# Optimization experiments

Hardware: AMD Instinct MI355X
Metric: run time of the kernel (lower is better)

The kernel has to match this reference:

```python
import jax, jax.numpy as jnp
import numpy as np

ALPHA = 32.0
LN_EPS = 1e-5

def _cdist(a, b):
    # a: [C, M, K], b: [C, N, K] -> [C, M, N] euclidean distances
    d2 = (jnp.sum(a * a, -1)[:, :, None]
          + jnp.sum(b * b, -1)[:, None, :]
          - 2.0 * jnp.einsum('cmk,cnk->cmn', a, b))
    return jnp.sqrt(jnp.maximum(d2, 1e-12))

def setup_inputs() -> dict:
    key = jax.random.key(0)
    k1, k2 = jax.random.split(key)
    B, D, H, W, C = 8, 16, 28, 28, 256
    CN, SS = 128, 28 * 28
    x = jax.random.normal(k1, (B, D, H, W, C), dtype=jnp.float32)
    ln_weight = jnp.ones((C,), dtype=jnp.float32)
    ln_bias = jnp.zeros((C,), dtype=jnp.float32)
    cluster_center = jax.random.uniform(k2, (C, CN, SS), dtype=jnp.float32)
    return {"x": x, "ln_weight": ln_weight, "ln_bias": ln_bias,
            "cluster_center": cluster_center}

def reference(x, ln_weight, ln_bias, cluster_center):
    B, D, H, W, C = x.shape
    CN = cluster_center.shape[1]
    # LayerNorm over last dim (feature_dim)
    mu = jnp.mean(x, -1, keepdims=True)
    var = jnp.mean(jnp.square(x - mu), -1, keepdims=True)
    xn = (x - mu) * jax.lax.rsqrt(var + LN_EPS) * ln_weight + ln_bias
    # B D H W C -> C (B D) (H W)
    x_re = jnp.transpose(xn, (4, 0, 1, 2, 3)).reshape(C, B * D, H * W)
    soft_assign = _cdist(x_re, cluster_center)          # [C, B*D, CN]
    # C (B D) CN -> B D C CN
    x_distance = jnp.transpose(soft_assign.reshape(C, B, D, CN), (1, 2, 0, 3))
    # NegSoftAssign: exp(-alpha*(x - min)) normalized == softmax(-alpha*x)
    x_distance_assign = jax.nn.softmax(-ALPHA * x_distance, axis=-1)
    cluster_dist = _cdist(cluster_center, cluster_center)  # [C, CN, CN]
    return (x_distance, x_distance_assign, cluster_dist)
```

## Files before the change

kernel.cpp:

```cpp
#include <hip/hip_runtime.h>
#include <hip/hip_bf16.h>
#include <math.h>

#define C_DIM 256
#define BD    128
#define HW    784
#define CN    128
#define KPAD  800

typedef short bf16x8 __attribute__((ext_vector_type(8)));
typedef float f32x4 __attribute__((ext_vector_type(4)));

__device__ inline ushort f2b(float f) {
  unsigned u = __float_as_uint(f);
  unsigned r = (u + 0x7FFFu + ((u >> 16) & 1u)) >> 16;
  return (ushort)r;
}

__global__ __launch_bounds__(256) void ln_transpose_kernel(
    const float* __restrict__ x, const float* __restrict__ lnw,
    const float* __restrict__ lnb, ushort* __restrict__ xre,
    float* __restrict__ anorm) {
  __shared__ ushort btile[256 * 36];
  __shared__ float nbuf[4][256];
  const int t = threadIdx.x, bd = blockIdx.y, bx = blockIdx.x;
  const int hw0 = bx * 32;
  const int w = t >> 6, lane = t & 63;
  const int q = lane >> 4, l = lane & 15;
  const bool last = (bx == 24);
  const int ngroups = last ? 1 : 2;
  const int rpw = ngroups * 4;
  if (last) {
    for (int r = 16; r < 32; ++r) btile[t * 36 + r] = 0;
  }
  float4 wv[4], bv[4];
  for (int s = 0; s < 4; ++s) {
    wv[s] = *(const float4*)(lnw + s * 64 + l * 4);
    bv[s] = *(const float4*)(lnb + s * 64 + l * 4);
  }
  float nrm[4][4];
  for (int s = 0; s < 4; ++s)
    for (int j = 0; j < 4; ++j) nrm[s][j] = 0.f;
  const float* xb = x + ((size_t)bd * HW + hw0) * 256 + l * 4;
  for (int g = 0; g < ngroups; ++g) {
    int r = w * rpw + g * 4 + q;
    float4 v[4];
    for (int s = 0; s < 4; ++s)
      v[s] = *(const float4*)(xb + (size_t)r * 256 + s * 64);
    float sum = 0.f, sq = 0.f;
    for (int s = 0; s < 4; ++s) {
      sum += v[s].x + v[s].y + v[s].z + v[s].w;
      sq = fmaf(v[s].x, v[s].x, sq); sq = fmaf(v[s].y, v[s].y, sq);
      sq = fmaf(v[s].z, v[s].z, sq); sq = fmaf(v[s].w, v[s].w, sq);
    }
    for (int off = 1; off <= 8; off <<= 1) {
      sum += __shfl_xor(sum, off, 64);
      sq  += __shfl_xor(sq, off, 64);
    }
    float mu = sum * (1.f / 256.f);
    float var = fmaf(-mu, mu, sq * (1.f / 256.f));
    float sc = rsqrtf(var + 1e-5f);
    for (int s = 0; s < 4; ++s) {
      float y0 = (v[s].x - mu) * sc * wv[s].x + bv[s].x;
      float y1 = (v[s].y - mu) * sc * wv[s].y + bv[s].y;
      float y2 = (v[s].z - mu) * sc * wv[s].z + bv[s].z;
      float y3 = (v[s].w - mu) * sc * wv[s].w + bv[s].w;
      nrm[s][0] = fmaf(y0, y0, nrm[s][0]);
      nrm[s][1] = fmaf(y1, y1, nrm[s][1]);
      nrm[s][2] = fmaf(y2, y2, nrm[s][2]);
      nrm[s][3] = fmaf(y3, y3, nrm[s][3]);
      int c = s * 64 + l * 4;
      btile[(c + 0) * 36 + r] = f2b(y0);
      btile[(c + 1) * 36 + r] = f2b(y1);
      btile[(c + 2) * 36 + r] = f2b(y2);
      btile[(c + 3) * 36 + r] = f2b(y3);
    }
  }
  for (int s = 0; s < 4; ++s)
    for (int j = 0; j < 4; ++j) {
      float v = nrm[s][j];
      v += __shfl_xor(v, 16, 64);
      v += __shfl_xor(v, 32, 64);
      nrm[s][j] = v;
    }
  if (q == 0)
    for (int s = 0; s < 4; ++s)
      for (int j = 0; j < 4; ++j) nbuf[w][s * 64 + l * 4 + j] = nrm[s][j];
  __syncthreads();
  float tot = nbuf[0][t] + nbuf[1][t] + nbuf[2][t] + nbuf[3][t];
  atomicAdd(&anorm[t * 128 + bd], tot);
  for (int i = 0; i < 8; ++i) {
    int c = w * 64 + i * 8 + (lane >> 3);
    int ho = (lane & 7) * 4;
    ushort4 val = *(const ushort4*)&btile[c * 36 + ho];
    *(ushort4*)(xre + (size_t)c * (BD * KPAD) + (size_t)bd * KPAD + hw0 + ho) = val;
  }
}

__global__ __launch_bounds__(256) void cc_convert_kernel(
    const float* __restrict__ cc, ushort* __restrict__ ccb,
    float* __restrict__ bnorm) {
  int b = blockIdx.x, c = b >> 3;
  int t = threadIdx.x, w = t >> 6, lane = t & 63;
  int q = lane >> 4, l = lane & 15;
  int r = (b & 7) * 16 + w * 4 + q;
  const float4* src = (const float4*)(cc + ((size_t)c * CN + r) * HW);
  ushort* dst = ccb + ((size_t)c * CN + r) * KPAD;
  float nrm = 0.f;
  for (int i = 0; i < 13; ++i) {
    int f = i * 16 + l;
    if (f < 196) {
      float4 v = src[f];
      nrm = fmaf(v.x, v.x, nrm); nrm = fmaf(v.y, v.y, nrm);
      nrm = fmaf(v.z, v.z, nrm); nrm = fmaf(v.w, v.w, nrm);
      ushort4 o; o.x = f2b(v.x); o.y = f2b(v.y); o.z = f2b(v.z); o.w = f2b(v.w);
      *(ushort4*)(dst + f * 4) = o;
    }
  }
  for (int off = 1; off <= 8; off <<= 1) nrm += __shfl_xor(nrm, off, 64);
  if (l == 0) bnorm[c * 128 + r] = nrm;
  if (l < 4) *(ushort4*)(dst + 784 + l * 4) = make_ushort4(0, 0, 0, 0);
}

__global__ __launch_bounds__(256, 2) void gemm_mfma_kernel(
    const ushort* __restrict__ xre, const ushort* __restrict__ ccb,
    const float* __restrict__ anorm, const float* __restrict__ bnorm,
    float* __restrict__ out_d, float* __restrict__ out_s,
    float* __restrict__ out_c) {
  __shared__ __align__(16) ushort At[2][4096];
  __shared__ __align__(16) ushort Bt[2][4096];
  __shared__ float smin[2][128];
  __shared__ float ssum[2][128];
  const int bx = blockIdx.x;
  const int c = bx >> 1, mode = bx & 1;
  const int t = threadIdx.x, w = t >> 6, lane = t & 63;
  const int quad = lane >> 4, ln = lane & 15;
  const int wrow = (w >> 1) * 64, wcol = (w & 1) * 64;
  const ushort* Ag = (mode ? ccb : xre) + (size_t)c * (128 * KPAD);
  const ushort* Bg = ccb + (size_t)c * (128 * KPAD);

  f32x4 acc[4][4];
  for (int i = 0; i < 4; ++i)
    for (int j = 0; j < 4; ++j) acc[i][j] = f32x4{0.f, 0.f, 0.f, 0.f};

  const int ci0 = 128 * w;
  const int row0 = (ci0 + lane) >> 2;
  const int row1 = (ci0 + 64 + lane) >> 2;
  const int q0 = (lane & 3) ^ (row0 & 3);
  const int q1 = (lane & 3) ^ (row1 & 3);
  const ushort* ga0 = Ag + (size_t)row0 * KPAD + q0 * 8;
  const ushort* ga1 = Ag + (size_t)row1 * KPAD + q1 * 8;
  const ushort* gb0 = Bg + (size_t)row0 * KPAD + q0 * 8;
  const ushort* gb1 = Bg + (size_t)row1 * KPAD + q1 * 8;
  const int la0 = ci0 * 8, la1 = (ci0 + 64) * 8;

#define ISSUE(k, p)                                                          \
  do {                                                                       \
    int kb = (k) * 32;                                                       \
    __builtin_amdgcn_global_load_lds(                                        \
        (const __attribute__((address_space(1))) unsigned int*)(ga0 + kb),   \
        (__attribute__((address_space(3))) unsigned int*)&At[p][la0], 16, 0, 0); \
    __builtin_amdgcn_global_load_lds(                                        \
        (const __attribute__((address_space(1))) unsigned int*)(ga1 + kb),   \
        (__attribute__((address_space(3))) unsigned int*)&At[p][la1], 16, 0, 0); \
    if (!mode) {                                                             \
      __builtin_amdgcn_global_load_lds(                                      \
          (const __attribute__((address_space(1))) unsigned int*)(gb0 + kb), \
          (__attribute__((address_space(3))) unsigned int*)&Bt[p][la0], 16, 0, 0); \
      __builtin_amdgcn_global_load_lds(                                      \
          (const __attribute__((address_space(1))) unsigned int*)(gb1 + kb), \
          (__attribute__((address_space(3))) unsigned int*)&Bt[p][la1], 16, 0, 0); \
    }                                                                        \
  } while (0)

  ISSUE(0, 0);
  for (int k0 = 0; k0 < 25; ++k0) {
    __syncthreads();
    if (k0 < 24) ISSUE(k0 + 1, (k0 + 1) & 1);
    const ushort* Ab = At[k0 & 1];
    const ushort* Bb = mode ? At[k0 & 1] : Bt[k0 & 1];
    bf16x8 af[4], bf[4];
    for (int i = 0; i < 4; ++i) {
      int m = wrow + i * 16 + ln;
      af[i] = *(const bf16x8*)&Ab[(m * 4 + (quad ^ (m & 3))) * 8];
    }
    for (int j = 0; j < 4; ++j) {
      int n = wcol + j * 16 + ln;
      bf[j] = *(const bf16x8*)&Bb[(n * 4 + (quad ^ (n & 3))) * 8];
    }
    for (int i = 0; i < 4; ++i)
      for (int j = 0; j < 4; ++j)
        acc[i][j] = __builtin_amdgcn_mfma_f32_16x16x32_bf16(af[i], bf[j], acc[i][j], 0, 0, 0);
  }
#undef ISSUE

  const float* rn = (mode ? bnorm : anorm) + c * 128;
  const float* cn = bnorm + c * 128;
  float cnv[4];
  for (int j = 0; j < 4; ++j) cnv[j] = cn[wcol + j * 16 + ln];
  float d[4][4][4];
  for (int i = 0; i < 4; ++i) {
    float rv[4];
    for (int r = 0; r < 4; ++r) rv[r] = rn[wrow + i * 16 + quad * 4 + r];
    for (int j = 0; j < 4; ++j)
      for (int r = 0; r < 4; ++r) {
        float d2 = rv[r] + cnv[j] - 2.f * acc[i][j][r];
        d[i][j][r] = sqrtf(fmaxf(d2, 1e-12f));
      }
  }

  if (mode) {
    float* ob = out_c + (size_t)c * (128 * 128);
    for (int i = 0; i < 4; ++i)
      for (int r = 0; r < 4; ++r) {
        int m = wrow + i * 16 + quad * 4 + r;
        for (int j = 0; j < 4; ++j) ob[m * 128 + wcol + j * 16 + ln] = d[i][j][r];
      }
  } else {
    int half = w & 1;
    for (int i = 0; i < 4; ++i)
      for (int r = 0; r < 4; ++r) {
        int m = wrow + i * 16 + quad * 4 + r;
        size_t ob = ((size_t)m * 256 + c) * 128 + wcol;
        for (int j = 0; j < 4; ++j) out_d[ob + j * 16 + ln] = d[i][j][r];
        float mn = fminf(fminf(d[i][0][r], d[i][1][r]), fminf(d[i][2][r], d[i][3][r]));
        for (int off = 1; off < 16; off <<= 1) mn = fminf(mn, __shfl_xor(mn, off, 64));
        if (ln == 0) smin[half][m] = mn;
      }
    __syncthreads();
    for (int i = 0; i < 4; ++i)
      for (int r = 0; r < 4; ++r) {
        int m = wrow + i * 16 + quad * 4 + r;
        float mn = fminf(smin[0][m], smin[1][m]);
        float s = 0.f;
        for (int j = 0; j < 4; ++j) {
          float e = __expf(-32.f * (d[i][j][r] - mn));
          d[i][j][r] = e;
          s += e;
        }
        for (int off = 1; off < 16; off <<= 1) s += __shfl_xor(s, off, 64);
        if (ln == 0) ssum[half][m] = s;
      }
    __syncthreads();
    for (int i = 0; i < 4; ++i)
      for (int r = 0; r < 4; ++r) {
        int m = wrow + i * 16 + quad * 4 + r;
        float inv = 1.f / (ssum[0][m] + ssum[1][m]);
        size_t ob = ((size_t)m * 256 + c) * 128 + wcol;
        for (int j = 0; j < 4; ++j) out_s[ob + j * 16 + ln] = d[i][j][r] * inv;
      }
  }
}

extern "C" void kernel_launch(void* const* d_in, const int* in_sizes, int n_in,
                              void* d_out, int out_size, void* d_ws, size_t ws_size,
                              hipStream_t stream) {
  const float* x   = (const float*)d_in[0];
  const float* lnw = (const float*)d_in[1];
  const float* lnb = (const float*)d_in[2];
  const float* cc  = (const float*)d_in[3];
  float* out   = (float*)d_out;
  float* out_d = out;
  float* out_s = out + 4194304;
  float* out_c = out + 8388608;

  ushort* xre_b = (ushort*)d_ws;
  ushort* cc_b  = xre_b + 26214400;
  float*  anorm = (float*)(cc_b + 26214400);
  float*  bnorm = anorm + 32768;

  hipMemsetAsync(anorm, 0, 32768 * sizeof(float), stream);
  ln_transpose_kernel<<<dim3(25, 128), 256, 0, stream>>>(x, lnw, lnb, xre_b, anorm);
  cc_convert_kernel<<<2048, 256, 0, stream>>>(cc, cc_b, bnorm);
  gemm_mfma_kernel<<<512, 256, 0, stream>>>(xre_b, cc_b, anorm, bnorm,
                                            out_d, out_s, out_c);
}
```

Measured before the change: 320.0 us.

## Split GEMM tiles by column half, move softmax to separate kernel, widen LN tiles

The GEMM grid doubles by giving each block half of the cluster columns. This cuts accumulators and shared memory so occupancy can rise to 4 blocks per CU, and 1024 blocks run instead of 512. The fused softmax, with its cross-wave min and sum reductions, moves into a separate row-wise kernel that re-reads out_d from global memory. The LN/transpose kernel now handles 64 spatial positions per block with an XOR-swizzled shared tile, and K is padded to 832. These changes trade an extra full read and write pass over the distance tensor for better GEMM parallelism and simpler epilogues.

```diff
diff --git a/kernel.cpp b/kernel.cpp
--- a/kernel.cpp
+++ b/kernel.cpp
@@ -6,7 +6,8 @@
 #define BD    128
 #define HW    784
 #define CN    128
-#define KPAD  800
+#define KPAD  832
+#define KTILES 26
 
 typedef short bf16x8 __attribute__((ext_vector_type(8)));
 typedef float f32x4 __attribute__((ext_vector_type(4)));
@@ -21,17 +22,18 @@
     const float* __restrict__ x, const float* __restrict__ lnw,
     const float* __restrict__ lnb, ushort* __restrict__ xre,
     float* __restrict__ anorm) {
-  __shared__ ushort btile[256 * 36];
+  __shared__ ushort btile[256 * 64];
   __shared__ float nbuf[4][256];
   const int t = threadIdx.x, bd = blockIdx.y, bx = blockIdx.x;
-  const int hw0 = bx * 32;
+  const int hw0 = bx * 64;
   const int w = t >> 6, lane = t & 63;
   const int q = lane >> 4, l = lane & 15;
-  const bool last = (bx == 24);
-  const int ngroups = last ? 1 : 2;
+  const bool last = (bx == 12);
+  const int ngroups = last ? 1 : 4;
   const int rpw = ngroups * 4;
   if (last) {
-    for (int r = 16; r < 32; ++r) btile[t * 36 + r] = 0;
+    for (int r = 16; r < 64; r += 4)
+      *(ushort4*)&btile[t * 64 + r] = make_ushort4(0, 0, 0, 0);
   }
   float4 wv[4], bv[4];
   for (int s = 0; s < 4; ++s) {
@@ -42,6 +44,7 @@
   for (int s = 0; s < 4; ++s)
     for (int j = 0; j < 4; ++j) nrm[s][j] = 0.f;
   const float* xb = x + ((size_t)bd * HW + hw0) * 256 + l * 4;
+  const int xr = l & 12;
   for (int g = 0; g < ngroups; ++g) {
     int r = w * rpw + g * 4 + q;
     float4 v[4];
@@ -60,6 +63,7 @@
     float mu = sum * (1.f / 256.f);
     float var = fmaf(-mu, mu, sq * (1.f / 256.f));
     float sc = rsqrtf(var + 1e-5f);
+    int rp = r ^ xr;
     for (int s = 0; s < 4; ++s) {
       float y0 = (v[s].x - mu) * sc * wv[s].x + bv[s].x;
       float y1 = (v[s].y - mu) * sc * wv[s].y + bv[s].y;
@@ -70,10 +74,10 @@
       nrm[s][2] = fmaf(y2, y2, nrm[s][2]);
       nrm[s][3] = fmaf(y3, y3, nrm[s][3]);
       int c = s * 64 + l * 4;
-      btile[(c + 0) * 36 + r] = f2b(y0);
-      btile[(c + 1) * 36 + r] = f2b(y1);
-      btile[(c + 2) * 36 + r] = f2b(y2);
-      btile[(c + 3) * 36 + r] = f2b(y3);
+      btile[(c + 0) * 64 + rp] = f2b(y0);
+      btile[(c + 1) * 64 + rp] = f2b(y1);
+      btile[(c + 2) * 64 + rp] = f2b(y2);
+      btile[(c + 3) * 64 + rp] = f2b(y3);
     }
   }
   for (int s = 0; s < 4; ++s)
@@ -89,11 +93,12 @@
   __syncthreads();
   float tot = nbuf[0][t] + nbuf[1][t] + nbuf[2][t] + nbuf[3][t];
   atomicAdd(&anorm[t * 128 + bd], tot);
-  for (int i = 0; i < 8; ++i) {
-    int c = w * 64 + i * 8 + (lane >> 3);
-    int ho = (lane & 7) * 4;
-    ushort4 val = *(const ushort4*)&btile[c * 36 + ho];
-    *(ushort4*)(xre + (size_t)c * (BD * KPAD) + (size_t)bd * KPAD + hw0 + ho) = val;
+  for (int i = 0; i < 16; ++i) {
+    int c = w * 64 + i * 4 + (lane >> 4);
+    int xw = (w * 16 + i) & 12;
+    int ho = (lane & 15) * 4;
+    uint2 val = *(const uint2*)&btile[c * 64 + (ho ^ xw)];
+    *(uint2*)(xre + (size_t)c * (BD * KPAD) + (size_t)bd * KPAD + hw0 + ho) = val;
   }
 }
 
@@ -119,137 +124,121 @@
   }
   for (int off = 1; off <= 8; off <<= 1) nrm += __shfl_xor(nrm, off, 64);
   if (l == 0) bnorm[c * 128 + r] = nrm;
-  if (l < 4) *(ushort4*)(dst + 784 + l * 4) = make_ushort4(0, 0, 0, 0);
-}
-
-__global__ __launch_bounds__(256, 2) void gemm_mfma_kernel(
+  if (l < 12) *(ushort4*)(dst + 784 + l * 4) = make_ushort4(0, 0, 0, 0);
+}
+
+__global__ __launch_bounds__(256, 4) void gemm_mfma_kernel(
     const ushort* __restrict__ xre, const ushort* __restrict__ ccb,
     const float* __restrict__ anorm, const float* __restrict__ bnorm,
-    float* __restrict__ out_d, float* __restrict__ out_s,
-    float* __restrict__ out_c) {
+    float* __restrict__ out_d, float* __restrict__ out_c) {
   __shared__ __align__(16) ushort At[2][4096];
-  __shared__ __align__(16) ushort Bt[2][4096];
-  __shared__ float smin[2][128];
-  __shared__ float ssum[2][128];
+  __shared__ __align__(16) ushort Bt[2][2048];
   const int bx = blockIdx.x;
-  const int c = bx >> 1, mode = bx & 1;
+  const int c = bx >> 2, mode = (bx >> 1) & 1, nh = bx & 1;
   const int t = threadIdx.x, w = t >> 6, lane = t & 63;
   const int quad = lane >> 4, ln = lane & 15;
-  const int wrow = (w >> 1) * 64, wcol = (w & 1) * 64;
   const ushort* Ag = (mode ? ccb : xre) + (size_t)c * (128 * KPAD);
-  const ushort* Bg = ccb + (size_t)c * (128 * KPAD);
-
-  f32x4 acc[4][4];
-  for (int i = 0; i < 4; ++i)
+  const ushort* Bg = ccb + (size_t)c * (128 * KPAD) + (size_t)(nh * 64) * KPAD;
+
+  f32x4 acc[2][4];
+  for (int i = 0; i < 2; ++i)
     for (int j = 0; j < 4; ++j) acc[i][j] = f32x4{0.f, 0.f, 0.f, 0.f};
 
-  const int ci0 = 128 * w;
-  const int row0 = (ci0 + lane) >> 2;
-  const int row1 = (ci0 + 64 + lane) >> 2;
-  const int q0 = (lane & 3) ^ (row0 & 3);
-  const int q1 = (lane & 3) ^ (row1 & 3);
-  const ushort* ga0 = Ag + (size_t)row0 * KPAD + q0 * 8;
-  const ushort* ga1 = Ag + (size_t)row1 * KPAD + q1 * 8;
-  const ushort* gb0 = Bg + (size_t)row0 * KPAD + q0 * 8;
-  const ushort* gb1 = Bg + (size_t)row1 * KPAD + q1 * 8;
-  const int la0 = ci0 * 8, la1 = (ci0 + 64) * 8;
-
-#define ISSUE(k, p)                                                          \
-  do {                                                                       \
-    int kb = (k) * 32;                                                       \
-    __builtin_amdgcn_global_load_lds(                                        \
-        (const __attribute__((address_space(1))) unsigned int*)(ga0 + kb),   \
-        (__attribute__((address_space(3))) unsigned int*)&At[p][la0], 16, 0, 0); \
-    __builtin_amdgcn_global_load_lds(                                        \
-        (const __attribute__((address_space(1))) unsigned int*)(ga1 + kb),   \
-        (__attribute__((address_space(3))) unsigned int*)&At[p][la1], 16, 0, 0); \
-    if (!mode) {                                                             \
-      __builtin_amdgcn_global_load_lds(                                      \
-          (const __attribute__((address_space(1))) unsigned int*)(gb0 + kb), \
-          (__attribute__((address_space(3))) unsigned int*)&Bt[p][la0], 16, 0, 0); \
-      __builtin_amdgcn_global_load_lds(                                      \
-          (const __attribute__((address_space(1))) unsigned int*)(gb1 + kb), \
-          (__attribute__((address_space(3))) unsigned int*)&Bt[p][la1], 16, 0, 0); \
-    }                                                                        \
+  const int ciA0 = w * 128 + lane, ciA1 = ciA0 + 64;
+  const int rowA0 = ciA0 >> 2, rowA1 = ciA1 >> 2;
+  const int qA0 = (ciA0 & 3) ^ (rowA0 & 3), qA1 = (ciA1 & 3) ^ (rowA1 & 3);
+  const ushort* gA0 = Ag + (size_t)rowA0 * KPAD + qA0 * 8;
+  const ushort* gA1 = Ag + (size_t)rowA1 * KPAD + qA1 * 8;
+  const int rowB = t >> 2, qB = (t & 3) ^ (rowB & 3);
+  const ushort* gB = Bg + (size_t)rowB * KPAD + qB * 8;
+
+#define ISSUE(k, p)                                                            \
+  do {                                                                         \
+    int kb = (k) * 32;                                                         \
+    __builtin_amdgcn_global_load_lds(                                          \
+        (const __attribute__((address_space(1))) unsigned int*)(gA0 + kb),     \
+        (__attribute__((address_space(3))) unsigned int*)&At[p][ciA0 * 8], 16, 0, 0); \
+    __builtin_amdgcn_global_load_lds(                                          \
+        (const __attribute__((address_space(1))) unsigned int*)(gA1 + kb),     \
+        (__attribute__((address_space(3))) unsigned int*)&At[p][ciA1 * 8], 16, 0, 0); \
+    if (!mode)                                                                 \
+      __builtin_amdgcn_global_load_lds(                                        \
+          (const __attribute__((address_space(1))) unsigned int*)(gB + kb),    \
+          (__attribute__((address_space(3))) unsigned int*)&Bt[p][t * 8], 16, 0, 0); \
   } while (0)
 
   ISSUE(0, 0);
-  for (int k0 = 0; k0 < 25; ++k0) {
+  for (int k0 = 0; k0 < KTILES; ++k0) {
     __syncthreads();
-    if (k0 < 24) ISSUE(k0 + 1, (k0 + 1) & 1);
-    const ushort* Ab = At[k0 & 1];
-    const ushort* Bb = mode ? At[k0 & 1] : Bt[k0 & 1];
-    bf16x8 af[4], bf[4];
-    for (int i = 0; i < 4; ++i) {
-      int m = wrow + i * 16 + ln;
+    if (k0 < KTILES - 1) ISSUE(k0 + 1, (k0 + 1) & 1);
+    const int p = k0 & 1;
+    const ushort* Ab = At[p];
+    bf16x8 af[2], bf[4];
+    for (int i = 0; i < 2; ++i) {
+      int m = w * 32 + i * 16 + ln;
       af[i] = *(const bf16x8*)&Ab[(m * 4 + (quad ^ (m & 3))) * 8];
     }
     for (int j = 0; j < 4; ++j) {
-      int n = wcol + j * 16 + ln;
-      bf[j] = *(const bf16x8*)&Bb[(n * 4 + (quad ^ (n & 3))) * 8];
-    }
-    for (int i = 0; i < 4; ++i)
+      int n = j * 16 + ln;
+      if (mode) {
+        int mr = nh * 64 + n;
+        bf[j] = *(const bf16x8*)&Ab[(mr * 4 + (quad ^ (mr & 3))) * 8];
+      } else {
+        bf[j] = *(const bf16x8*)&Bt[p][(n * 4 + (quad ^ (n & 3))) * 8];
+      }
+    }
+    for (int i = 0; i < 2; ++i)
       for (int j = 0; j < 4; ++j)
         acc[i][j] = __builtin_amdgcn_mfma_f32_16x16x32_bf16(af[i], bf[j], acc[i][j], 0, 0, 0);
   }
 #undef ISSUE
 
   const float* rn = (mode ? bnorm : anorm) + c * 128;
-  const float* cn = bnorm + c * 128;
+  const float* cnp = bnorm + c * 128 + nh * 64;
   float cnv[4];
-  for (int j = 0; j < 4; ++j) cnv[j] = cn[wcol + j * 16 + ln];
-  float d[4][4][4];
-  for (int i = 0; i < 4; ++i) {
+  for (int j = 0; j < 4; ++j) cnv[j] = cnp[j * 16 + ln];
+  for (int i = 0; i < 2; ++i) {
     float rv[4];
-    for (int r = 0; r < 4; ++r) rv[r] = rn[wrow + i * 16 + quad * 4 + r];
-    for (int j = 0; j < 4; ++j)
-      for (int r = 0; r < 4; ++r) {
+    for (int r = 0; r < 4; ++r) rv[r] = rn[w * 32 + i * 16 + quad * 4 + r];
+    for (int r = 0; r < 4; ++r) {
+      int m = w * 32 + i * 16 + quad * 4 + r;
+      float dr[4];
+      for (int j = 0; j < 4; ++j) {
         float d2 = rv[r] + cnv[j] - 2.f * acc[i][j][r];
-        d[i][j][r] = sqrtf(fmaxf(d2, 1e-12f));
+        dr[j] = sqrtf(fmaxf(d2, 1e-12f));
       }
-  }
-
-  if (mode) {
-    float* ob = out_c + (size_t)c * (128 * 128);
-    for (int i = 0; i < 4; ++i)
-      for (int r = 0; r < 4; ++r) {
-        int m = wrow + i * 16 + quad * 4 + r;
-        for (int j = 0; j < 4; ++j) ob[m * 128 + wcol + j * 16 + ln] = d[i][j][r];
+      if (mode) {
+        float* ob = out_c + (size_t)c * (128 * 128) + (size_t)m * 128 + nh * 64;
+        for (int j = 0; j < 4; ++j) ob[j * 16 + ln] = dr[j];
+      } else {
+        float* ob = out_d + ((size_t)m * 256 + c) * 128 + nh * 64;
+        for (int j = 0; j < 4; ++j) ob[j * 16 + ln] = dr[j];
       }
-  } else {
-    int half = w & 1;
-    for (int i = 0; i < 4; ++i)
-      for (int r = 0; r < 4; ++r) {
-        int m = wrow + i * 16 + quad * 4 + r;
-        size_t ob = ((size_t)m * 256 + c) * 128 + wcol;
-        for (int j = 0; j < 4; ++j) out_d[ob + j * 16 + ln] = d[i][j][r];
-        float mn = fminf(fminf(d[i][0][r], d[i][1][r]), fminf(d[i][2][r], d[i][3][r]));
-        for (int off = 1; off < 16; off <<= 1) mn = fminf(mn, __shfl_xor(mn, off, 64));
-        if (ln == 0) smin[half][m] = mn;
-      }
-    __syncthreads();
-    for (int i = 0; i < 4; ++i)
-      for (int r = 0; r < 4; ++r) {
-        int m = wrow + i * 16 + quad * 4 + r;
-        float mn = fminf(smin[0][m], smin[1][m]);
-        float s = 0.f;
-        for (int j = 0; j < 4; ++j) {
-          float e = __expf(-32.f * (d[i][j][r] - mn));
-          d[i][j][r] = e;
-          s += e;
-        }
-        for (int off = 1; off < 16; off <<= 1) s += __shfl_xor(s, off, 64);
-        if (ln == 0) ssum[half][m] = s;
-      }
-    __syncthreads();
-    for (int i = 0; i < 4; ++i)
-      for (int r = 0; r < 4; ++r) {
-        int m = wrow + i * 16 + quad * 4 + r;
-        float inv = 1.f / (ssum[0][m] + ssum[1][m]);
-        size_t ob = ((size_t)m * 256 + c) * 128 + wcol;
-        for (int j = 0; j < 4; ++j) out_s[ob + j * 16 + ln] = d[i][j][r] * inv;
-      }
-  }
+    }
+  }
+}
+
+__global__ __launch_bounds__(256) void softmax_kernel(
+    const float* __restrict__ out_d, float* __restrict__ out_s) {
+  const int t = threadIdx.x, w = t >> 6, lane = t & 63;
+  const int q = lane >> 4, l = lane & 15;
+  const int row = blockIdx.x * 16 + w * 4 + q;
+  const float4* src = (const float4*)(out_d + (size_t)row * 128);
+  float4 v0 = src[l], v1 = src[l + 16];
+  float mn = fminf(fminf(fminf(v0.x, v0.y), fminf(v0.z, v0.w)),
+                   fminf(fminf(v1.x, v1.y), fminf(v1.z, v1.w)));
+  for (int off = 1; off <= 8; off <<= 1) mn = fminf(mn, __shfl_xor(mn, off, 64));
+  float e[8];
+  e[0] = __expf(-32.f * (v0.x - mn)); e[1] = __expf(-32.f * (v0.y - mn));
+  e[2] = __expf(-32.f * (v0.z - mn)); e[3] = __expf(-32.f * (v0.w - mn));
+  e[4] = __expf(-32.f * (v1.x - mn)); e[5] = __expf(-32.f * (v1.y - mn));
+  e[6] = __expf(-32.f * (v1.z - mn)); e[7] = __expf(-32.f * (v1.w - mn));
+  float s = e[0] + e[1] + e[2] + e[3] + e[4] + e[5] + e[6] + e[7];
+  for (int off = 1; off <= 8; off <<= 1) s += __shfl_xor(s, off, 64);
+  float inv = 1.f / s;
+  float4* dst = (float4*)(out_s + (size_t)row * 128);
+  dst[l]      = make_float4(e[0] * inv, e[1] * inv, e[2] * inv, e[3] * inv);
+  dst[l + 16] = make_float4(e[4] * inv, e[5] * inv, e[6] * inv, e[7] * inv);
 }
 
 extern "C" void kernel_launch(void* const* d_in, const int* in_sizes, int n_in,
@@ -265,13 +254,13 @@
   float* out_c = out + 8388608;
 
   ushort* xre_b = (ushort*)d_ws;
-  ushort* cc_b  = xre_b + 26214400;
-  float*  anorm = (float*)(cc_b + 26214400);
+  ushort* cc_b  = xre_b + 27262976;
+  float*  anorm = (float*)(cc_b + 27262976);
   float*  bnorm = anorm + 32768;
 
   hipMemsetAsync(anorm, 0, 32768 * sizeof(float), stream);
-  ln_transpose_kernel<<<dim3(25, 128), 256, 0, stream>>>(x, lnw, lnb, xre_b, anorm);
+  ln_transpose_kernel<<<dim3(13, 128), 256, 0, stream>>>(x, lnw, lnb, xre_b, anorm);
   cc_convert_kernel<<<2048, 256, 0, stream>>>(cc, cc_b, bnorm);
-  gemm_mfma_kernel<<<512, 256, 0, stream>>>(xre_b, cc_b, anorm, bnorm,
-                                            out_d, out_s, out_c);
-}
+  gemm_mfma_kernel<<<1024, 256, 0, stream>>>(xre_b, cc_b, anorm, bnorm, out_d, out_c);
+  softmax_kernel<<<2048, 256, 0, stream>>>(out_d, out_s);
+}
```

New measurement: 315.3 us. Within noise of the previous version (-1.5%).
